# Kernel tuning notes

Hardware: AMD Instinct MI355X
Metric: run time of the kernel (lower is better)

The kernel has to match this reference:

```python
import jax, jax.numpy as jnp
import numpy as np

N, E, G = 16000, 256000, 64
H, NR, L = 128, 96, 2
CUTOFF = 6.0
EPS = 1e-10

def _ln(x, eps=1e-5):
    m = jnp.mean(x, -1, keepdims=True)
    v = jnp.mean((x - m) ** 2, -1, keepdims=True)
    return (x - m) * jax.lax.rsqrt(v + eps)

def _mlp2(x, w1, b1, w2, b2):
    return jax.nn.silu(x @ w1 + b1) @ w2 + b2

def _xav(key, shape):
    s = (2.0 / (shape[-2] + shape[-1])) ** 0.5
    return jax.random.normal(key, shape, jnp.float32) * s

def setup_inputs():
    key = jax.random.key(0)
    ks = iter(jax.random.split(key, 64))
    pos = jax.random.normal(next(ks), (N, 3), jnp.float32) * 2.0
    z = jax.random.randint(next(ks), (N,), 1, 95)
    batch = jnp.sort(jax.random.randint(next(ks), (N,), 0, G))
    src = jax.random.randint(next(ks), (E,), 0, N)
    off = jax.random.randint(next(ks), (E,), 1, N)
    dst = (src + off) % N  # no self loops -> dist > 0
    edge_index = jnp.stack([src, dst]).astype(jnp.int32)
    H3 = 3 * H
    return dict(
        pos=pos,
        z_emb_w=jax.random.normal(next(ks), (95, H), jnp.float32),
        ne_emb_w=jax.random.normal(next(ks), (95, H), jnp.float32),
        rl_w1=_xav(next(ks), (NR, H)), rl_b1=jnp.zeros((H,), jnp.float32),
        rl_w2=_xav(next(ks), (H, H)), rl_b2=jnp.zeros((H,), jnp.float32),
        sv_w=_xav(next(ks), (H, H)), sv_b=jnp.zeros((H,), jnp.float32),
        lin_w1=_xav(next(ks), (3, H // 4)), lin_b1=jnp.zeros((H // 4,), jnp.float32),
        lin_w2=_xav(next(ks), (H // 4, 1)), lin_b2=jnp.zeros((1,), jnp.float32),
        mp_ln_g=jnp.ones((L, H), jnp.float32), mp_ln_b=jnp.zeros((L, H), jnp.float32),
        mp_xw1=_xav(next(ks), (L, H, H)), mp_xb1=jnp.zeros((L, H), jnp.float32),
        mp_xw2=_xav(next(ks), (L, H, H3)), mp_xb2=jnp.zeros((L, H3), jnp.float32),
        mp_rw=_xav(next(ks), (L, NR, H3)), mp_rb=jnp.zeros((L, H3), jnp.float32),
        mp_dw1=_xav(next(ks), (L, H3 + NR, H3)), mp_db1=jnp.zeros((L, H3), jnp.float32),
        mp_dw2=_xav(next(ks), (L, H3, H3)), mp_db2=jnp.zeros((L, H3), jnp.float32),
        ft_vw=_xav(next(ks), (L, H, 2 * H)),
        ft_xw1=_xav(next(ks), (L, 2 * H, H)), ft_xb1=jnp.zeros((L, H), jnp.float32),
        ft_xw2=_xav(next(ks), (L, H, H3)), ft_xb2=jnp.zeros((L, H3), jnp.float32),
        last_w=_xav(next(ks), (H, 1)), last_b=jnp.zeros((1,), jnp.float32),
        z=z, edge_index=edge_index, batch=batch,
    )

def _forward(pos, z_emb_w, ne_emb_w, rl_w1, rl_b1, rl_w2, rl_b2, sv_w, sv_b,
             lin_w1, lin_b1, lin_w2, lin_b2, mp_ln_g, mp_ln_b, mp_xw1, mp_xb1,
             mp_xw2, mp_xb2, mp_rw, mp_rb, mp_dw1, mp_db1, mp_dw2, mp_db2,
             ft_vw, ft_xw1, ft_xb1, ft_xw2, ft_xb2, last_w, last_b,
             z, edge_index, batch):
    inv_sqrt3 = 1.0 / (3.0 ** 0.5)
    inv_sqrt_h = 1.0 / (H ** 0.5)
    inv_sqrt2 = 1.0 / (2.0 ** 0.5)
    src, dst = edge_index[0], edge_index[1]  # gather from src, scatter-add to dst
    edge_vec = pos[src] - pos[dst]                         # (E,3)
    dist = jnp.sqrt(jnp.sum(edge_vec ** 2, -1))            # (E,)
    # rbf_emb buffers
    start = jnp.exp(jnp.float32(-CUTOFF))
    means = jnp.linspace(start, 1.0, NR)
    betas = (2.0 / NR * (1.0 - start)) ** (-2.0)
    d = dist[:, None]
    rbounds = 0.5 * (jnp.cos(dist * jnp.pi / CUTOFF) + 1.0) * (dist < CUTOFF).astype(dist.dtype)
    rbf = rbounds[:, None] * jnp.exp(-betas * (jnp.exp(-d) - means) ** 2)   # (E,NR)
    rh = rbounds[:, None] * _mlp2(rbf, rl_w1, rl_b1, rl_w2, rl_b2)          # (E,H) radial_hidden
    # embeddings + NeighborEmb (gather-scale-scatter)
    s = _ln(z_emb_w[z])
    sn = _ln(ne_emb_w[z])
    s = s + jax.ops.segment_sum(rh * sn[src], dst, num_segments=N)
    vec = jnp.zeros((N, 3, H), pos.dtype)
    # edge-wise equivariant frame
    edge_diff = edge_vec / d
    edge_cross = jnp.cross(pos[src], pos[dst])
    edge_cross = edge_cross / (jnp.linalg.norm(edge_cross, axis=-1, keepdims=True) + EPS)
    edge_vertical = jnp.cross(edge_diff, edge_cross)
    edge_frame = jnp.stack([edge_diff, edge_cross, edge_vertical], -1)      # (E,3,3)
    # S_vector
    s1 = jax.nn.silu(_ln(s @ sv_w + sv_b))
    msgv = (rh[:, None, :] * edge_diff[:, :, None]) * s1[src][:, None, :]   # (E,3,H)
    S_ij = jax.ops.segment_sum(msgv, dst, num_segments=N)                   # (N,3,H)

    def _scalarize(Sg):
        sc = jnp.einsum('eck,ech->ekh', edge_frame, Sg)    # (E,3,H)
        sc = sc.at[:, 1, :].set(jnp.abs(sc[:, 1, :]))
        p = jnp.transpose(sc, (0, 2, 1))                   # (E,H,3)
        out = _mlp2(p, lin_w1, lin_b1, lin_w2, lin_b2) + p[:, :, 0:1]
        return out[..., 0]                                 # (E,H)

    scalar3 = _scalarize(S_ij[src])
    scalar4 = _scalarize(S_ij[dst])
    edge_weight = jnp.concatenate([scalar3, scalar4], -1) * rbounds[:, None]
    edge_weight = jnp.concatenate([edge_weight, rh, rbf], -1)  # (E, 3H+NR)

    for l in range(L):
        # EquiMessagePassing
        xh = _mlp2(mp_ln_g[l] * _ln(s) + mp_ln_b[l], mp_xw1[l], mp_xb1[l], mp_xw2[l], mp_xb2[l])  # (N,3H)
        rbfh = (rbf @ mp_rw[l] + mp_rb[l]) * _mlp2(edge_weight, mp_dw1[l], mp_db1[l], mp_dw2[l], mp_db2[l])
        m = xh[src] * rbfh                                  # (E,3H)
        mx, m2, m3 = jnp.split(m, 3, -1)
        m2 = m2 * inv_sqrt3
        mvec = (vec[src] * m2[:, None, :] + m3[:, None, :] * edge_diff[:, :, None]) * inv_sqrt_h
        s = (s + jax.ops.segment_sum(mx, dst, num_segments=N)) * inv_sqrt2
        vec = vec + jax.ops.segment_sum(mvec, dst, num_segments=N)
        # FTE (node_frame unused by FTE in the original code)
        vp = jnp.einsum('nch,hk->nck', vec, ft_vw[l])       # (N,3,2H)
        v1, v2 = jnp.split(vp, 2, -1)
        scalar = jnp.sqrt(jnp.sum(v1 ** 2, 1) + 1e-10)      # (N,H)
        vec_dot = jnp.sum(v1 * v2, 1) * inv_sqrt_h
        xvh = _mlp2(jnp.concatenate([s, scalar], -1), ft_xw1[l], ft_xb1[l], ft_xw2[l], ft_xb2[l])
        x1, x2, x3 = jnp.split(xvh, 3, -1)
        s = s + (x1 + x2 + vec_dot) * inv_sqrt2
        vec = vec + x3[:, None, :] * v2

    out = s @ last_w + last_b                               # (N,1)
    return jax.ops.segment_sum(out, batch, num_segments=G)  # (G,1) sum readout

def reference(pos, z_emb_w, ne_emb_w, rl_w1, rl_b1, rl_w2, rl_b2, sv_w, sv_b,
              lin_w1, lin_b1, lin_w2, lin_b2, mp_ln_g, mp_ln_b, mp_xw1, mp_xb1,
              mp_xw2, mp_xb2, mp_rw, mp_rb, mp_dw1, mp_db1, mp_dw2, mp_db2,
              ft_vw, ft_xw1, ft_xb1, ft_xw2, ft_xb2, last_w, last_b,
              z, edge_index, batch):
    return _forward(pos, z_emb_w, ne_emb_w, rl_w1, rl_b1, rl_w2, rl_b2, sv_w, sv_b,
                    lin_w1, lin_b1, lin_w2, lin_b2, mp_ln_g, mp_ln_b, mp_xw1, mp_xb1,
                    mp_xw2, mp_xb2, mp_rw, mp_rb, mp_dw1, mp_db1, mp_dw2, mp_db2,
                    ft_vw, ft_xw1, ft_xb1, ft_xw2, ft_xb2, last_w, last_b,
                    z, edge_index, batch)
```

## Files before the change

kernel.cpp:

```cpp
#include <hip/hip_runtime.h>
#include <math.h>

#define NN 16000
#define NE 256000
#define NG 64
#define HD 128
#define NRAD 96
#define H3 384
#define KD 480

typedef unsigned short u16;
typedef short short8 __attribute__((ext_vector_type(8)));
typedef float f32x4 __attribute__((ext_vector_type(4)));

__device__ __forceinline__ float siluf(float x){ return x / (1.0f + expf(-x)); }

__device__ __forceinline__ float wsum(float v){
#pragma unroll
    for (int o = 32; o > 0; o >>= 1) v += __shfl_xor(v, o, 64);
    return v;
}

__device__ __forceinline__ u16 f2bh(float f){
    unsigned int u = __float_as_uint(f);
    unsigned int r = u + 0x7FFFu + ((u >> 16) & 1u);
    return (u16)(r >> 16);
}
__device__ __forceinline__ float bh2f(u16 h){
    return __uint_as_float((unsigned int)h << 16);
}
__device__ __forceinline__ short8 ld8(const u16* p){ return *(const short8*)p; }

__global__ void k_fill(float* __restrict__ p, float v, int n){
    int i = blockIdx.x * blockDim.x + threadIdx.x;
    if (i < n) p[i] = v;
}

__global__ void k_wsplit(const float* __restrict__ src, u16* __restrict__ dh, u16* __restrict__ dl,
                         int K, int N){
    int i = blockIdx.x * 256 + threadIdx.x;
    if (i >= K * N) return;
    int n = i / K, k = i - n * K;
    float v = src[(size_t)k * N + n];
    u16 h = f2bh(v);
    dh[i] = h;
    dl[i] = f2bh(v - bh2f(h));
}

__global__ void k_node_embed(const float* __restrict__ zw, const float* __restrict__ nw,
                             const int* __restrict__ z, float* __restrict__ s, float* __restrict__ sn){
    int n = blockIdx.x, t = threadIdx.x;
    int zi = z[n];
    const float* a = zw + (size_t)zi * HD;
    const float* b = nw + (size_t)zi * HD;
    float a0 = a[t], a1 = a[t + 64];
    float m  = wsum(a0 + a1) * (1.f / HD);
    float va = wsum((a0 - m)*(a0 - m) + (a1 - m)*(a1 - m)) * (1.f / HD);
    float r  = rsqrtf(va + 1e-5f);
    s[(size_t)n*HD + t]      = (a0 - m) * r;
    s[(size_t)n*HD + 64 + t] = (a1 - m) * r;
    float b0 = b[t], b1 = b[t + 64];
    m  = wsum(b0 + b1) * (1.f / HD);
    va = wsum((b0 - m)*(b0 - m) + (b1 - m)*(b1 - m)) * (1.f / HD);
    r  = rsqrtf(va + 1e-5f);
    sn[(size_t)n*HD + t]      = (b0 - m) * r;
    sn[(size_t)n*HD + 64 + t] = (b1 - m) * r;
}

__global__ void k_ln_silu(const float* __restrict__ x, float* __restrict__ out){
    int n = blockIdx.x, t = threadIdx.x;
    float a0 = x[(size_t)n*HD + t], a1 = x[(size_t)n*HD + 64 + t];
    float m  = wsum(a0 + a1) * (1.f / HD);
    float va = wsum((a0 - m)*(a0 - m) + (a1 - m)*(a1 - m)) * (1.f / HD);
    float r  = rsqrtf(va + 1e-5f);
    out[(size_t)n*HD + t]      = siluf((a0 - m) * r);
    out[(size_t)n*HD + 64 + t] = siluf((a1 - m) * r);
}

__global__ void k_ln_aff(const float* __restrict__ x, const float* __restrict__ g,
                         const float* __restrict__ b, float* __restrict__ out){
    int n = blockIdx.x, t = threadIdx.x;
    float a0 = x[(size_t)n*HD + t], a1 = x[(size_t)n*HD + 64 + t];
    float m  = wsum(a0 + a1) * (1.f / HD);
    float va = wsum((a0 - m)*(a0 - m) + (a1 - m)*(a1 - m)) * (1.f / HD);
    float r  = rsqrtf(va + 1e-5f);
    out[(size_t)n*HD + t]      = g[t]      * ((a0 - m) * r) + b[t];
    out[(size_t)n*HD + 64 + t] = g[64 + t] * ((a1 - m) * r) + b[64 + t];
}

__global__ void k_edge_geom(const float* __restrict__ pos, const int* __restrict__ ei,
                            float* __restrict__ dist, float* __restrict__ rbnd,
                            float* __restrict__ frame){
    int e = blockIdx.x * blockDim.x + threadIdx.x;
    if (e >= NE) return;
    int si = ei[e], di = ei[NE + e];
    float sx = pos[si*3], sy = pos[si*3+1], sz = pos[si*3+2];
    float dx = pos[di*3], dy = pos[di*3+1], dz = pos[di*3+2];
    float vx = sx - dx, vy = sy - dy, vz = sz - dz;
    float dd = sqrtf(vx*vx + vy*vy + vz*vz);
    dist[e] = dd;
    float rb = (dd < 6.0f) ? 0.5f * (cosf(dd * 0.5235987755982988f) + 1.0f) : 0.0f;
    rbnd[e] = rb;
    float inv = 1.0f / dd;
    float ux = vx*inv, uy = vy*inv, uz = vz*inv;
    float cx = sy*dz - sz*dy, cy = sz*dx - sx*dz, cz = sx*dy - sy*dx;
    float cn = sqrtf(cx*cx + cy*cy + cz*cz) + 1e-10f;
    cx /= cn; cy /= cn; cz /= cn;
    float wx = uy*cz - uz*cy, wy = uz*cx - ux*cz, wz = ux*cy - uy*cx;
    frame[(0*3+0)*NE + e] = ux; frame[(1*3+0)*NE + e] = uy; frame[(2*3+0)*NE + e] = uz;
    frame[(0*3+1)*NE + e] = cx; frame[(1*3+1)*NE + e] = cy; frame[(2*3+1)*NE + e] = cz;
    frame[(0*3+2)*NE + e] = wx; frame[(1*3+2)*NE + e] = wy; frame[(2*3+2)*NE + e] = wz;
}

__global__ void k_rbf(const float* __restrict__ dist, const float* __restrict__ rbnd,
                      float* __restrict__ base, int e0, int ec){
    int idx = blockIdx.x * 256 + threadIdx.x;
    int e = idx / NRAD;
    if (e >= ec) return;
    int k = idx - e * NRAD;
    int eg = e0 + e;
    float start = expf(-6.0f);
    float mean  = start + (1.0f - start) * ((float)k / 95.0f);
    float c     = (2.0f / 96.0f) * (1.0f - start);
    float betas = 1.0f / (c * c);
    float t = expf(-dist[eg]) - mean;
    base[(size_t)e * KD + k] = rbnd[eg] * expf(-betas * t * t);
}

__global__ __launch_bounds__(256)
void mgemm(const float* __restrict__ A, int lda,
           const u16* __restrict__ Bhg, const u16* __restrict__ Blg, int K,
           const float* __restrict__ bias, int act,
           float* __restrict__ C, int ldc,
           int M, int Nn,
           const float* __restrict__ row_scale,
           const float* __restrict__ mulC, int ldm){
    __shared__ u16 Ah[128*40], Al[128*40];
    __shared__ u16 Bh[64*40],  Bl[64*40];
    int tid = threadIdx.x;
    int w = tid >> 6, l = tid & 63;
    int row0 = blockIdx.x * 128, col0 = blockIdx.y * 64;
    f32x4 acc[2][4] = {};
    const int r16 = l & 15, kb = (l >> 4) * 8;

    for (int k0 = 0; k0 < K; k0 += 32){
        if (k0) __syncthreads();
#pragma unroll
        for (int i = 0; i < 4; i++){
            int f = tid + i * 256;
            int r = f >> 3, kq = (f & 7) * 4;
            const float4 v = *(const float4*)(A + (size_t)(row0 + r) * lda + k0 + kq);
            u16 h0 = f2bh(v.x), h1 = f2bh(v.y), h2 = f2bh(v.z), h3 = f2bh(v.w);
            u16 g0 = f2bh(v.x - bh2f(h0)), g1 = f2bh(v.y - bh2f(h1));
            u16 g2 = f2bh(v.z - bh2f(h2)), g3 = f2bh(v.w - bh2f(h3));
            uint2 ph, pl;
            ph.x = (unsigned)h0 | ((unsigned)h1 << 16); ph.y = (unsigned)h2 | ((unsigned)h3 << 16);
            pl.x = (unsigned)g0 | ((unsigned)g1 << 16); pl.y = (unsigned)g2 | ((unsigned)g3 << 16);
            *(uint2*)&Ah[r*40 + kq] = ph;
            *(uint2*)&Al[r*40 + kq] = pl;
        }
        {
            int bn = tid >> 2, kq = (tid & 3) * 8;
            const size_t gb = (size_t)(col0 + bn) * K + k0 + kq;
            *(short8*)&Bh[bn*40 + kq] = ld8(Bhg + gb);
            *(short8*)&Bl[bn*40 + kq] = ld8(Blg + gb);
        }
        __syncthreads();
        short8 ah0 = *(const short8*)&Ah[(w*32      + r16)*40 + kb];
        short8 ah1 = *(const short8*)&Ah[(w*32 + 16 + r16)*40 + kb];
        short8 al0 = *(const short8*)&Al[(w*32      + r16)*40 + kb];
        short8 al1 = *(const short8*)&Al[(w*32 + 16 + r16)*40 + kb];
#pragma unroll
        for (int nf = 0; nf < 4; nf++){
            short8 bhv = *(const short8*)&Bh[(nf*16 + r16)*40 + kb];
            short8 blv = *(const short8*)&Bl[(nf*16 + r16)*40 + kb];
            acc[0][nf] = __builtin_amdgcn_mfma_f32_16x16x32_bf16(ah0, bhv, acc[0][nf], 0, 0, 0);
            acc[0][nf] = __builtin_amdgcn_mfma_f32_16x16x32_bf16(al0, bhv, acc[0][nf], 0, 0, 0);
            acc[0][nf] = __builtin_amdgcn_mfma_f32_16x16x32_bf16(ah0, blv, acc[0][nf], 0, 0, 0);
            acc[1][nf] = __builtin_amdgcn_mfma_f32_16x16x32_bf16(ah1, bhv, acc[1][nf], 0, 0, 0);
            acc[1][nf] = __builtin_amdgcn_mfma_f32_16x16x32_bf16(al1, bhv, acc[1][nf], 0, 0, 0);
            acc[1][nf] = __builtin_amdgcn_mfma_f32_16x16x32_bf16(ah1, blv, acc[1][nf], 0, 0, 0);
        }
    }
    int rq = (l >> 4) * 4;
#pragma unroll
    for (int mf = 0; mf < 2; mf++){
#pragma unroll
        for (int nf = 0; nf < 4; nf++){
            int n = col0 + nf*16 + r16;
            float bz = bias ? bias[n] : 0.0f;
#pragma unroll
            for (int reg = 0; reg < 4; reg++){
                int m = row0 + w*32 + mf*16 + rq + reg;
                float v = acc[mf][nf][reg] + bz;
                if (act) v = siluf(v);
                if (row_scale) v *= row_scale[m];
                if (mulC) v *= mulC[(size_t)m * ldm + n];
                C[(size_t)m * ldc + n] = v;
            }
        }
    }
}

struct WT { u16* h; u16* l; };

static void gemm(hipStream_t st, const float* A, int lda, WT B,
                 const float* bias, float* C, int ldc, size_t M, int K, int Nn,
                 int act, const float* rs, const float* mul, int ldm){
    dim3 g((unsigned)(M / 128), (unsigned)(Nn / 64)), b(256);
    mgemm<<<g, b, 0, st>>>(A, lda, B.h, B.l, K, bias, act, C, ldc, (int)M, Nn, rs, mul, ldm);
}

__global__ void k_scatter_s(const float* __restrict__ rh, const float* __restrict__ sn,
                            const int* __restrict__ ei, float* __restrict__ s, int e0, int ec){
    int idx = blockIdx.x * 256 + threadIdx.x;
    int e = idx >> 7, h = idx & 127;
    if (e >= ec) return;
    int eg = e0 + e;
    int si = ei[eg], di = ei[NE + eg];
    atomicAdd(&s[(size_t)di * HD + h], rh[(size_t)e * KD + h] * sn[(size_t)si * HD + h]);
}

__global__ void k_scatter_msgv(const float* __restrict__ rh, const float* __restrict__ s1,
                               const float* __restrict__ frame, const int* __restrict__ ei,
                               float* __restrict__ S_ij, int e0, int ec){
    int idx = blockIdx.x * 256 + threadIdx.x;
    int e = idx >> 7, h = idx & 127;
    if (e >= ec) return;
    int eg = e0 + e;
    int si = ei[eg], di = ei[NE + eg];
    float mv = rh[(size_t)e * KD + h] * s1[(size_t)si * HD + h];
    size_t db = (size_t)di * H3;
#pragma unroll
    for (int c = 0; c < 3; c++){
        float df = frame[(c*3 + 0) * NE + eg];
        atomicAdd(&S_ij[db + c * HD + h], mv * df);
    }
}

__global__ void k_scalarize(const float* __restrict__ S_ij, const float* __restrict__ frame,
                            const float* __restrict__ rbnd, const int* __restrict__ ei,
                            const float* __restrict__ w1, const float* __restrict__ b1,
                            const float* __restrict__ w2, const float* __restrict__ b2v,
                            float* __restrict__ base, int e0){
    int e = blockIdx.x, h = threadIdx.x;
    int eg = e0 + e;
    int si = ei[eg], di = ei[NE + eg];
    float fr[9];
#pragma unroll
    for (int i = 0; i < 9; i++) fr[i] = frame[i * NE + eg];
    float rb = rbnd[eg];
    float b2 = b2v[0];
#pragma unroll
    for (int g = 0; g < 2; g++){
        int node = g ? di : si;
        float S0 = S_ij[(size_t)node * H3 + h];
        float S1 = S_ij[(size_t)node * H3 + 128 + h];
        float S2 = S_ij[(size_t)node * H3 + 256 + h];
        float p0 = fr[0]*S0 + fr[3]*S1 + fr[6]*S2;
        float p1 = fabsf(fr[1]*S0 + fr[4]*S1 + fr[7]*S2);
        float p2 = fr[2]*S0 + fr[5]*S1 + fr[8]*S2;
        float o = b2 + p0;
#pragma unroll
        for (int j = 0; j < 32; j++){
            float hh = siluf(p0 * w1[j] + p1 * w1[32 + j] + p2 * w1[64 + j] + b1[j]);
            o += hh * w2[j];
        }
        base[(size_t)e * KD + g * 128 + h] = o * rb;
    }
}

__global__ void k_scatter_layer(const float* __restrict__ rbfh, const float* __restrict__ xh,
                                const float* __restrict__ vec, const float* __restrict__ frame,
                                const int* __restrict__ ei, float* __restrict__ s,
                                float* __restrict__ vec_acc, int e0, int ec){
    int idx = blockIdx.x * 256 + threadIdx.x;
    int e = idx >> 7, h = idx & 127;
    if (e >= ec) return;
    int eg = e0 + e;
    int si = ei[eg], di = ei[NE + eg];
    size_t eb = (size_t)e * H3, sb = (size_t)si * H3, db = (size_t)di * H3;
    float mx = xh[sb + h]       * rbfh[eb + h];
    float m2 = xh[sb + 128 + h] * rbfh[eb + 128 + h] * 0.5773502691896258f;
    float m3 = xh[sb + 256 + h] * rbfh[eb + 256 + h];
    atomicAdd(&s[(size_t)di * HD + h], mx);
#pragma unroll
    for (int c = 0; c < 3; c++){
        float df = frame[(c*3 + 0) * NE + eg];
        float mv = (vec[sb + c * HD + h] * m2 + m3 * df) * 0.08838834764831845f;
        atomicAdd(&vec_acc[db + c * HD + h], mv);
    }
}

__global__ void k_scale_s(float* __restrict__ s){
    int i = blockIdx.x * 256 + threadIdx.x;
    s[i] *= 0.7071067811865476f;
}

__global__ void k_vec_add(float* __restrict__ vec, const float* __restrict__ vec_acc){
    int i = blockIdx.x * 256 + threadIdx.x;
    vec[i] += vec_acc[i];
}

__global__ void k_vfeat(const float* __restrict__ vp, const float* __restrict__ s,
                        float* __restrict__ t256, float* __restrict__ vdot){
    int idx = blockIdx.x * 256 + threadIdx.x;
    int n = idx >> 7, h = idx & 127;
    float a = 0.f, b = 0.f;
#pragma unroll
    for (int c = 0; c < 3; c++){
        float v1 = vp[(size_t)(n*3 + c) * 256 + h];
        float v2 = vp[(size_t)(n*3 + c) * 256 + 128 + h];
        a += v1 * v1;
        b += v1 * v2;
    }
    t256[(size_t)n * 256 + 128 + h] = sqrtf(a + 1e-10f);
    vdot[idx] = b * 0.08838834764831845f;
    t256[(size_t)n * 256 + h] = s[idx];
}

__global__ void k_upd_s(float* __restrict__ s, const float* __restrict__ xvh,
                        const float* __restrict__ vdot){
    int idx = blockIdx.x * 256 + threadIdx.x;
    int n = idx >> 7, h = idx & 127;
    s[idx] += (xvh[(size_t)n * H3 + h] + xvh[(size_t)n * H3 + 128 + h] + vdot[idx]) * 0.7071067811865476f;
}

__global__ void k_upd_vec(float* __restrict__ vec, const float* __restrict__ xvh,
                          const float* __restrict__ vp){
    int idx = blockIdx.x * 256 + threadIdx.x;
    int n = idx / H3;
    int r = idx - n * H3;
    int c = r >> 7, h = r & 127;
    vec[idx] += xvh[(size_t)n * H3 + 256 + h] * vp[(size_t)(n*3 + c) * 256 + 128 + h];
}

__global__ void k_final(const float* __restrict__ s, const float* __restrict__ lw,
                        const float* __restrict__ lb, const int* __restrict__ batch,
                        float* __restrict__ out){
    int n = blockIdx.x, t = threadIdx.x;
    float v = s[(size_t)n * HD + t] * lw[t] + s[(size_t)n * HD + 64 + t] * lw[64 + t];
    v = wsum(v);
    if (t == 0) atomicAdd(&out[batch[n]], v + lb[0]);
}

extern "C" void kernel_launch(void* const* d_in, const int* in_sizes, int n_in,
                              void* d_out, int out_size, void* d_ws, size_t ws_size,
                              hipStream_t stream){
    const float* pos      = (const float*)d_in[0];
    const float* z_emb_w  = (const float*)d_in[1];
    const float* ne_emb_w = (const float*)d_in[2];
    const float* rl_w1    = (const float*)d_in[3];
    const float* rl_b1    = (const float*)d_in[4];
    const float* rl_w2    = (const float*)d_in[5];
    const float* rl_b2    = (const float*)d_in[6];
    const float* sv_w     = (const float*)d_in[7];
    const float* sv_b     = (const float*)d_in[8];
    const float* lin_w1   = (const float*)d_in[9];
    const float* lin_b1   = (const float*)d_in[10];
    const float* lin_w2   = (const float*)d_in[11];
    const float* lin_b2   = (const float*)d_in[12];
    const float* mp_ln_g  = (const float*)d_in[13];
    const float* mp_ln_b  = (const float*)d_in[14];
    const float* mp_xw1   = (const float*)d_in[15];
    const float* mp_xb1   = (const float*)d_in[16];
    const float* mp_xw2   = (const float*)d_in[17];
    const float* mp_xb2   = (const float*)d_in[18];
    const float* mp_rw    = (const float*)d_in[19];
    const float* mp_rb    = (const float*)d_in[20];
    const float* mp_dw1   = (const float*)d_in[21];
    const float* mp_db1   = (const float*)d_in[22];
    const float* mp_dw2   = (const float*)d_in[23];
    const float* mp_db2   = (const float*)d_in[24];
    const float* ft_vw    = (const float*)d_in[25];
    const float* ft_xw1   = (const float*)d_in[26];
    const float* ft_xb1   = (const float*)d_in[27];
    const float* ft_xw2   = (const float*)d_in[28];
    const float* ft_xb2   = (const float*)d_in[29];
    const float* last_w   = (const float*)d_in[30];
    const float* last_b   = (const float*)d_in[31];
    const int*   z        = (const int*)d_in[32];
    const int*   ei       = (const int*)d_in[33];
    const int*   batch    = (const int*)d_in[34];
    float* out = (float*)d_out;
    (void)in_sizes; (void)n_in; (void)out_size;

    float* ws = (float*)d_ws;
    size_t off = 0;
    auto alloc = [&](size_t nf){ float* p = ws + off; off += (nf + 63) & ~(size_t)63; return p; };

    float* s       = alloc((size_t)NN * HD);
    float* sn      = alloc((size_t)NN * HD);
    float* s1      = alloc((size_t)NN * HD);
    float* tA      = alloc((size_t)NN * HD);
    float* vdot    = alloc((size_t)NN * HD);
    float* vec     = alloc((size_t)NN * H3);
    float* vec_acc = alloc((size_t)NN * H3);
    float* S_ij    = alloc((size_t)NN * H3);
    float* xh      = alloc((size_t)NN * H3);
    float* vp      = alloc((size_t)NN * 3 * 256);
    float* dist    = alloc((size_t)NE);
    float* rbnd    = alloc((size_t)NE);
    float* frame   = alloc((size_t)NE * 9);
    float* t256    = sn;

    const size_t WELEMS = 45056 + 2 * 548864;
    u16* wcur = (u16*)alloc(WELEMS);
    auto wsplit = [&](const float* src, int K, int N)->WT{
        WT r; r.h = wcur; wcur += (size_t)K * N; r.l = wcur; wcur += (size_t)K * N;
        k_wsplit<<<(unsigned)(((size_t)K * N + 255) / 256), 256, 0, stream>>>(src, r.h, r.l, K, N);
        return r;
    };
    WT W_rl1 = wsplit(rl_w1, NRAD, HD);
    WT W_rl2 = wsplit(rl_w2, HD, HD);
    WT W_sv  = wsplit(sv_w, HD, HD);
    WT W_xw1[2], W_xw2[2], W_rw[2], W_dw1[2], W_dw2[2], W_vw[2], W_fx1[2], W_fx2[2];
    for (int l = 0; l < 2; l++){
        W_xw1[l] = wsplit(mp_xw1 + (size_t)l * HD * HD, HD, HD);
        W_xw2[l] = wsplit(mp_xw2 + (size_t)l * HD * H3, HD, H3);
        W_rw[l]  = wsplit(mp_rw  + (size_t)l * NRAD * H3, NRAD, H3);
        W_dw1[l] = wsplit(mp_dw1 + (size_t)l * KD * H3, KD, H3);
        W_dw2[l] = wsplit(mp_dw2 + (size_t)l * H3 * H3, H3, H3);
        W_vw[l]  = wsplit(ft_vw  + (size_t)l * HD * 256, HD, 256);
        W_fx1[l] = wsplit(ft_xw1 + (size_t)l * 256 * HD, 256, HD);
        W_fx2[l] = wsplit(ft_xw2 + (size_t)l * HD * H3, HD, H3);
    }

    size_t availF = ws_size / sizeof(float);
    size_t rem = (availF > off) ? (availF - off) : 0;
    const size_t EWF = (size_t)NE * KD;
    bool persist;
    size_t CE;
    float* ew  = nullptr;
    float* ewc = nullptr;
    if (rem >= EWF + 2 * (size_t)16000 * H3 + 256){
        persist = true;
        ew = alloc(EWF);
        size_t ce = (rem - EWF - 256) / (2 * (size_t)H3);
        CE = ce & ~(size_t)127;
        if (CE > NE) CE = NE;
    } else {
        persist = false;
        size_t ce = (rem > 256) ? (rem - 256) / ((size_t)KD + 2 * (size_t)H3) : 128;
        CE = ce & ~(size_t)127;
        if (CE < 128) CE = 128;
        if (CE > NE) CE = NE;
    }
    if (CE > 32768) CE = 32768;
    if (!persist) ewc = alloc(CE * KD);
    float* rbuf = alloc(CE * H3);
    float* hbuf = alloc(CE * H3);

    auto build_rh = [&](size_t e0, size_t ec, float* base){
        k_rbf<<<(unsigned)((ec * NRAD) / 256), 256, 0, stream>>>(dist, rbnd, base + 384, (int)e0, (int)ec);
        gemm(stream, base + 384, KD, W_rl1, rl_b1, hbuf, HD, ec, NRAD, HD, 1, nullptr, nullptr, 0);
        gemm(stream, hbuf, HD, W_rl2, rl_b2, base + 256, KD, ec, HD, HD, 0, rbnd + e0, nullptr, 0);
    };

    k_fill<<<1, 64, 0, stream>>>(out, 0.f, NG);
    k_node_embed<<<NN, 64, 0, stream>>>(z_emb_w, ne_emb_w, z, s, sn);
    k_edge_geom<<<NE / 256, 256, 0, stream>>>(pos, ei, dist, rbnd, frame);

    for (size_t e0 = 0; e0 < NE; e0 += CE){
        size_t ec = (NE - e0 < CE) ? (NE - e0) : CE;
        float* base = persist ? (ew + e0 * KD) : ewc;
        build_rh(e0, ec, base);
        k_scatter_s<<<(unsigned)((ec * HD) / 256), 256, 0, stream>>>(base + 256, sn, ei, s, (int)e0, (int)ec);
    }

    gemm(stream, s, HD, W_sv, sv_b, tA, HD, NN, HD, HD, 0, nullptr, nullptr, 0);
    k_ln_silu<<<NN, 64, 0, stream>>>(tA, s1);

    k_fill<<<(NN * H3) / 256, 256, 0, stream>>>(S_ij, 0.f, NN * H3);
    for (size_t e0 = 0; e0 < NE; e0 += CE){
        size_t ec = (NE - e0 < CE) ? (NE - e0) : CE;
        float* base = persist ? (ew + e0 * KD) : ewc;
        if (!persist) build_rh(e0, ec, base);
        k_scatter_msgv<<<(unsigned)((ec * HD) / 256), 256, 0, stream>>>(base + 256, s1, frame, ei, S_ij, (int)e0, (int)ec);
    }

    if (persist)
        k_scalarize<<<NE, 128, 0, stream>>>(S_ij, frame, rbnd, ei, lin_w1, lin_b1, lin_w2, lin_b2, ew, 0);

    k_fill<<<(NN * H3) / 256, 256, 0, stream>>>(vec, 0.f, NN * H3);

    for (int l = 0; l < 2; l++){
        k_ln_aff<<<NN, 64, 0, stream>>>(s, mp_ln_g + l * HD, mp_ln_b + l * HD, tA);
        gemm(stream, tA, HD, W_xw1[l], mp_xb1 + l * HD, vdot, HD, NN, HD, HD, 1, nullptr, nullptr, 0);
        gemm(stream, vdot, HD, W_xw2[l], mp_xb2 + l * H3, xh, H3, NN, HD, H3, 0, nullptr, nullptr, 0);

        k_fill<<<(NN * H3) / 256, 256, 0, stream>>>(vec_acc, 0.f, NN * H3);

        for (size_t e0 = 0; e0 < NE; e0 += CE){
            size_t ec = (NE - e0 < CE) ? (NE - e0) : CE;
            float* base = persist ? (ew + e0 * KD) : ewc;
            if (!persist){
                build_rh(e0, ec, base);
                k_scalarize<<<(unsigned)ec, 128, 0, stream>>>(S_ij, frame, rbnd, ei, lin_w1, lin_b1, lin_w2, lin_b2, base, (int)e0);
            }
            gemm(stream, base + 384, KD, W_rw[l], mp_rb + l * H3, rbuf, H3, ec, NRAD, H3, 0, nullptr, nullptr, 0);
            gemm(stream, base, KD, W_dw1[l], mp_db1 + l * H3, hbuf, H3, ec, KD, H3, 1, nullptr, nullptr, 0);
            gemm(stream, hbuf, H3, W_dw2[l], mp_db2 + l * H3, rbuf, H3, ec, H3, H3, 0, nullptr, rbuf, H3);
            k_scatter_layer<<<(unsigned)((ec * HD) / 256), 256, 0, stream>>>(rbuf, xh, vec, frame, ei, s, vec_acc, (int)e0, (int)ec);
        }
        k_scale_s<<<(NN * HD) / 256, 256, 0, stream>>>(s);
        k_vec_add<<<(NN * H3) / 256, 256, 0, stream>>>(vec, vec_acc);

        gemm(stream, vec, HD, W_vw[l], nullptr, vp, 256, (size_t)NN * 3, HD, 256, 0, nullptr, nullptr, 0);
        k_vfeat<<<(NN * HD) / 256, 256, 0, stream>>>(vp, s, t256, vdot);

        gemm(stream, t256, 256, W_fx1[l], ft_xb1 + l * HD, tA, HD, NN, 256, HD, 1, nullptr, nullptr, 0);
        gemm(stream, tA, HD, W_fx2[l], ft_xb2 + l * H3, xh, H3, NN, HD, H3, 0, nullptr, nullptr, 0);

        k_upd_s<<<(NN * HD) / 256, 256, 0, stream>>>(s, xh, vdot);
        k_upd_vec<<<(NN * H3) / 256, 256, 0, stream>>>(vec, xh, vp);
    }

    k_final<<<NN, 64, 0, stream>>>(s, last_w, last_b, batch, out);
}
```

Baseline: 12.41 ms.

## Enlarge GEMM tile to 128x128 and prefetch next K-slice into registers

The split-bf16 MFMA GEMM now uses 128x128 output tiles with a 2x2 warp layout, so each warp computes a 64x64 sub-tile of 4x4 fragments instead of 32x64. This raises MFMA work per shared-memory fragment load and halves the redundant A-tile conversion across column blocks. Global loads for the next K step are issued into registers before the current step's MFMAs, overlapping memory latency with compute. The cost is higher register pressure (64 accumulator vectors plus prefetch buffers), which may lower occupancy. Any Nn not divisible by 128 (e.g. 96) would also break.

```diff
diff --git a/kernel.cpp b/kernel.cpp
--- a/kernel.cpp
+++ b/kernel.cpp
@@ -136,62 +136,87 @@
            const float* __restrict__ row_scale,
            const float* __restrict__ mulC, int ldm){
     __shared__ u16 Ah[128*40], Al[128*40];
-    __shared__ u16 Bh[64*40],  Bl[64*40];
+    __shared__ u16 Bh[128*40], Bl[128*40];
     int tid = threadIdx.x;
     int w = tid >> 6, l = tid & 63;
-    int row0 = blockIdx.x * 128, col0 = blockIdx.y * 64;
-    f32x4 acc[2][4] = {};
-    const int r16 = l & 15, kb = (l >> 4) * 8;
-
+    int wm = w >> 1, wn = w & 1;
+    int r16 = l & 15, kb = (l >> 4) * 8, rq = (l >> 4) * 4;
+    int row0 = blockIdx.x * 128, col0 = blockIdx.y * 128;
+
+    int ar[4], akq[4];
+    const float* agp[4];
+#pragma unroll
+    for (int i = 0; i < 4; i++){
+        int f = tid + i * 256;
+        ar[i] = f >> 3; akq[i] = (f & 7) * 4;
+        agp[i] = A + (size_t)(row0 + ar[i]) * lda + akq[i];
+    }
+    int bn = tid >> 1, bkq = (tid & 1) * 16;
+    const u16* bgp_h = Bhg + (size_t)(col0 + bn) * K + bkq;
+    const u16* bgp_l = Blg + (size_t)(col0 + bn) * K + bkq;
+
+    float4 va[4];
+    short8 vbh0, vbh1, vbl0, vbl1;
+#pragma unroll
+    for (int i = 0; i < 4; i++) va[i] = *(const float4*)(agp[i]);
+    vbh0 = ld8(bgp_h); vbh1 = ld8(bgp_h + 8);
+    vbl0 = ld8(bgp_l); vbl1 = ld8(bgp_l + 8);
+
+    f32x4 acc[4][4] = {};
     for (int k0 = 0; k0 < K; k0 += 32){
         if (k0) __syncthreads();
 #pragma unroll
         for (int i = 0; i < 4; i++){
-            int f = tid + i * 256;
-            int r = f >> 3, kq = (f & 7) * 4;
-            const float4 v = *(const float4*)(A + (size_t)(row0 + r) * lda + k0 + kq);
+            float4 v = va[i];
             u16 h0 = f2bh(v.x), h1 = f2bh(v.y), h2 = f2bh(v.z), h3 = f2bh(v.w);
             u16 g0 = f2bh(v.x - bh2f(h0)), g1 = f2bh(v.y - bh2f(h1));
             u16 g2 = f2bh(v.z - bh2f(h2)), g3 = f2bh(v.w - bh2f(h3));
             uint2 ph, pl;
             ph.x = (unsigned)h0 | ((unsigned)h1 << 16); ph.y = (unsigned)h2 | ((unsigned)h3 << 16);
             pl.x = (unsigned)g0 | ((unsigned)g1 << 16); pl.y = (unsigned)g2 | ((unsigned)g3 << 16);
-            *(uint2*)&Ah[r*40 + kq] = ph;
-            *(uint2*)&Al[r*40 + kq] = pl;
-        }
-        {
-            int bn = tid >> 2, kq = (tid & 3) * 8;
-            const size_t gb = (size_t)(col0 + bn) * K + k0 + kq;
-            *(short8*)&Bh[bn*40 + kq] = ld8(Bhg + gb);
-            *(short8*)&Bl[bn*40 + kq] = ld8(Blg + gb);
-        }
+            *(uint2*)&Ah[ar[i]*40 + akq[i]] = ph;
+            *(uint2*)&Al[ar[i]*40 + akq[i]] = pl;
+        }
+        *(short8*)&Bh[bn*40 + bkq]     = vbh0;
+        *(short8*)&Bh[bn*40 + bkq + 8] = vbh1;
+        *(short8*)&Bl[bn*40 + bkq]     = vbl0;
+        *(short8*)&Bl[bn*40 + bkq + 8] = vbl1;
         __syncthreads();
-        short8 ah0 = *(const short8*)&Ah[(w*32      + r16)*40 + kb];
-        short8 ah1 = *(const short8*)&Ah[(w*32 + 16 + r16)*40 + kb];
-        short8 al0 = *(const short8*)&Al[(w*32      + r16)*40 + kb];
-        short8 al1 = *(const short8*)&Al[(w*32 + 16 + r16)*40 + kb];
+        if (k0 + 32 < K){
+#pragma unroll
+            for (int i = 0; i < 4; i++) va[i] = *(const float4*)(agp[i] + k0 + 32);
+            vbh0 = ld8(bgp_h + k0 + 32); vbh1 = ld8(bgp_h + k0 + 40);
+            vbl0 = ld8(bgp_l + k0 + 32); vbl1 = ld8(bgp_l + k0 + 40);
+        }
+        short8 fah[4], fal[4], fbh[4], fbl[4];
+#pragma unroll
+        for (int mf = 0; mf < 4; mf++){
+            fah[mf] = *(const short8*)&Ah[(wm*64 + mf*16 + r16)*40 + kb];
+            fal[mf] = *(const short8*)&Al[(wm*64 + mf*16 + r16)*40 + kb];
+        }
 #pragma unroll
         for (int nf = 0; nf < 4; nf++){
-            short8 bhv = *(const short8*)&Bh[(nf*16 + r16)*40 + kb];
-            short8 blv = *(const short8*)&Bl[(nf*16 + r16)*40 + kb];
-            acc[0][nf] = __builtin_amdgcn_mfma_f32_16x16x32_bf16(ah0, bhv, acc[0][nf], 0, 0, 0);
-            acc[0][nf] = __builtin_amdgcn_mfma_f32_16x16x32_bf16(al0, bhv, acc[0][nf], 0, 0, 0);
-            acc[0][nf] = __builtin_amdgcn_mfma_f32_16x16x32_bf16(ah0, blv, acc[0][nf], 0, 0, 0);
-            acc[1][nf] = __builtin_amdgcn_mfma_f32_16x16x32_bf16(ah1, bhv, acc[1][nf], 0, 0, 0);
-            acc[1][nf] = __builtin_amdgcn_mfma_f32_16x16x32_bf16(al1, bhv, acc[1][nf], 0, 0, 0);
-            acc[1][nf] = __builtin_amdgcn_mfma_f32_16x16x32_bf16(ah1, blv, acc[1][nf], 0, 0, 0);
-        }
-    }
-    int rq = (l >> 4) * 4;
-#pragma unroll
-    for (int mf = 0; mf < 2; mf++){
+            fbh[nf] = *(const short8*)&Bh[(wn*64 + nf*16 + r16)*40 + kb];
+            fbl[nf] = *(const short8*)&Bl[(wn*64 + nf*16 + r16)*40 + kb];
+        }
+#pragma unroll
+        for (int mf = 0; mf < 4; mf++)
+#pragma unroll
+            for (int nf = 0; nf < 4; nf++){
+                acc[mf][nf] = __builtin_amdgcn_mfma_f32_16x16x32_bf16(fah[mf], fbh[nf], acc[mf][nf], 0, 0, 0);
+                acc[mf][nf] = __builtin_amdgcn_mfma_f32_16x16x32_bf16(fal[mf], fbh[nf], acc[mf][nf], 0, 0, 0);
+                acc[mf][nf] = __builtin_amdgcn_mfma_f32_16x16x32_bf16(fah[mf], fbl[nf], acc[mf][nf], 0, 0, 0);
+            }
+    }
+#pragma unroll
+    for (int mf = 0; mf < 4; mf++){
 #pragma unroll
         for (int nf = 0; nf < 4; nf++){
-            int n = col0 + nf*16 + r16;
+            int n = col0 + wn*64 + nf*16 + r16;
             float bz = bias ? bias[n] : 0.0f;
 #pragma unroll
             for (int reg = 0; reg < 4; reg++){
-                int m = row0 + w*32 + mf*16 + rq + reg;
+                int m = row0 + wm*64 + mf*16 + rq + reg;
                 float v = acc[mf][nf][reg] + bz;
                 if (act) v = siluf(v);
                 if (row_scale) v *= row_scale[m];
@@ -207,7 +232,7 @@
 static void gemm(hipStream_t st, const float* A, int lda, WT B,
                  const float* bias, float* C, int ldc, size_t M, int K, int Nn,
                  int act, const float* rs, const float* mul, int ldm){
-    dim3 g((unsigned)(M / 128), (unsigned)(Nn / 64)), b(256);
+    dim3 g((unsigned)(M / 128), (unsigned)(Nn / 128)), b(256);
     mgemm<<<g, b, 0, st>>>(A, lda, B.h, B.l, K, bias, act, C, ldc, (int)M, Nn, rs, mul, ldm);
 }
 
```

Result: slower. 12.67 ms (+2.1%).

## Fuse radial GEMM, dw2 GEMM and edge scatter into one kernel

Applied to the files above, without the earlier changes.

Adds a kernel that computes the rbf-to-H3 GEMM and the second dense GEMM in the same tile, multiplies them with the biases, and does the atomic scatter into s and vec_acc in its epilogue. This drops the rbuf intermediate and the separate scatter kernel, removing two full edge×384 write/read round trips per chunk. Workspace sizing is reworked so chunks can grow larger without the former 32768 cap. The cost is a heavier epilogue with scattered atomics and gathers laid out per MFMA fragment, which is less coalesced than the old per-h scatter.

```diff
diff --git a/kernel.cpp b/kernel.cpp
--- a/kernel.cpp
+++ b/kernel.cpp
@@ -202,6 +202,144 @@
     }
 }
 
+__global__ __launch_bounds__(256)
+void dw2s(const float* __restrict__ hb,
+          const float* __restrict__ ewrbf,
+          const u16* __restrict__ B1h, const u16* __restrict__ B1l,
+          const u16* __restrict__ B2h, const u16* __restrict__ B2l,
+          const float* __restrict__ rb, const float* __restrict__ db2,
+          const float* __restrict__ xh, const float* __restrict__ vec,
+          const float* __restrict__ frame, const int* __restrict__ ei,
+          float* __restrict__ s, float* __restrict__ vec_acc, int e0){
+    __shared__ u16 Ah[128*40], Al[128*40];
+    __shared__ u16 Bh[64*40],  Bl[64*40];
+    int tid = threadIdx.x;
+    int w = tid >> 6, l = tid & 63;
+    int row0 = blockIdx.x * 128, col0 = blockIdx.y * 64;
+    const int r16 = l & 15, kb = (l >> 4) * 8;
+    f32x4 acc1[2][4] = {}, acc2[2][4] = {};
+
+    for (int k0 = 0; k0 < 96; k0 += 32){
+        if (k0) __syncthreads();
+#pragma unroll
+        for (int i = 0; i < 4; i++){
+            int f = tid + i * 256;
+            int r = f >> 3, kq = (f & 7) * 4;
+            const float4 v = *(const float4*)(ewrbf + (size_t)(row0 + r) * KD + k0 + kq);
+            u16 h0 = f2bh(v.x), h1 = f2bh(v.y), h2 = f2bh(v.z), h3 = f2bh(v.w);
+            u16 g0 = f2bh(v.x - bh2f(h0)), g1 = f2bh(v.y - bh2f(h1));
+            u16 g2 = f2bh(v.z - bh2f(h2)), g3 = f2bh(v.w - bh2f(h3));
+            uint2 ph, pl;
+            ph.x = (unsigned)h0 | ((unsigned)h1 << 16); ph.y = (unsigned)h2 | ((unsigned)h3 << 16);
+            pl.x = (unsigned)g0 | ((unsigned)g1 << 16); pl.y = (unsigned)g2 | ((unsigned)g3 << 16);
+            *(uint2*)&Ah[r*40 + kq] = ph;
+            *(uint2*)&Al[r*40 + kq] = pl;
+        }
+        {
+            int bn = tid >> 2, kq = (tid & 3) * 8;
+            const size_t gb = (size_t)(col0 + bn) * 96 + k0 + kq;
+            *(short8*)&Bh[bn*40 + kq] = ld8(B2h + gb);
+            *(short8*)&Bl[bn*40 + kq] = ld8(B2l + gb);
+        }
+        __syncthreads();
+        short8 ah0 = *(const short8*)&Ah[(w*32      + r16)*40 + kb];
+        short8 ah1 = *(const short8*)&Ah[(w*32 + 16 + r16)*40 + kb];
+        short8 al0 = *(const short8*)&Al[(w*32      + r16)*40 + kb];
+        short8 al1 = *(const short8*)&Al[(w*32 + 16 + r16)*40 + kb];
+#pragma unroll
+        for (int nf = 0; nf < 4; nf++){
+            short8 bhv = *(const short8*)&Bh[(nf*16 + r16)*40 + kb];
+            short8 blv = *(const short8*)&Bl[(nf*16 + r16)*40 + kb];
+            acc2[0][nf] = __builtin_amdgcn_mfma_f32_16x16x32_bf16(ah0, bhv, acc2[0][nf], 0, 0, 0);
+            acc2[0][nf] = __builtin_amdgcn_mfma_f32_16x16x32_bf16(al0, bhv, acc2[0][nf], 0, 0, 0);
+            acc2[0][nf] = __builtin_amdgcn_mfma_f32_16x16x32_bf16(ah0, blv, acc2[0][nf], 0, 0, 0);
+            acc2[1][nf] = __builtin_amdgcn_mfma_f32_16x16x32_bf16(ah1, bhv, acc2[1][nf], 0, 0, 0);
+            acc2[1][nf] = __builtin_amdgcn_mfma_f32_16x16x32_bf16(al1, bhv, acc2[1][nf], 0, 0, 0);
+            acc2[1][nf] = __builtin_amdgcn_mfma_f32_16x16x32_bf16(ah1, blv, acc2[1][nf], 0, 0, 0);
+        }
+    }
+    for (int k0 = 0; k0 < H3; k0 += 32){
+        __syncthreads();
+#pragma unroll
+        for (int i = 0; i < 4; i++){
+            int f = tid + i * 256;
+            int r = f >> 3, kq = (f & 7) * 4;
+            const float4 v = *(const float4*)(hb + (size_t)(row0 + r) * H3 + k0 + kq);
+            u16 h0 = f2bh(v.x), h1 = f2bh(v.y), h2 = f2bh(v.z), h3 = f2bh(v.w);
+            u16 g0 = f2bh(v.x - bh2f(h0)), g1 = f2bh(v.y - bh2f(h1));
+            u16 g2 = f2bh(v.z - bh2f(h2)), g3 = f2bh(v.w - bh2f(h3));
+            uint2 ph, pl;
+            ph.x = (unsigned)h0 | ((unsigned)h1 << 16); ph.y = (unsigned)h2 | ((unsigned)h3 << 16);
+            pl.x = (unsigned)g0 | ((unsigned)g1 << 16); pl.y = (unsigned)g2 | ((unsigned)g3 << 16);
+            *(uint2*)&Ah[r*40 + kq] = ph;
+            *(uint2*)&Al[r*40 + kq] = pl;
+        }
+        {
+            int bn = tid >> 2, kq = (tid & 3) * 8;
+            const size_t gb = (size_t)(col0 + bn) * H3 + k0 + kq;
+            *(short8*)&Bh[bn*40 + kq] = ld8(B1h + gb);
+            *(short8*)&Bl[bn*40 + kq] = ld8(B1l + gb);
+        }
+        __syncthreads();
+        short8 ah0 = *(const short8*)&Ah[(w*32      + r16)*40 + kb];
+        short8 ah1 = *(const short8*)&Ah[(w*32 + 16 + r16)*40 + kb];
+        short8 al0 = *(const short8*)&Al[(w*32      + r16)*40 + kb];
+        short8 al1 = *(const short8*)&Al[(w*32 + 16 + r16)*40 + kb];
+#pragma unroll
+        for (int nf = 0; nf < 4; nf++){
+            short8 bhv = *(const short8*)&Bh[(nf*16 + r16)*40 + kb];
+            short8 blv = *(const short8*)&Bl[(nf*16 + r16)*40 + kb];
+            acc1[0][nf] = __builtin_amdgcn_mfma_f32_16x16x32_bf16(ah0, bhv, acc1[0][nf], 0, 0, 0);
+            acc1[0][nf] = __builtin_amdgcn_mfma_f32_16x16x32_bf16(al0, bhv, acc1[0][nf], 0, 0, 0);
+            acc1[0][nf] = __builtin_amdgcn_mfma_f32_16x16x32_bf16(ah0, blv, acc1[0][nf], 0, 0, 0);
+            acc1[1][nf] = __builtin_amdgcn_mfma_f32_16x16x32_bf16(ah1, bhv, acc1[1][nf], 0, 0, 0);
+            acc1[1][nf] = __builtin_amdgcn_mfma_f32_16x16x32_bf16(al1, bhv, acc1[1][nf], 0, 0, 0);
+            acc1[1][nf] = __builtin_amdgcn_mfma_f32_16x16x32_bf16(ah1, blv, acc1[1][nf], 0, 0, 0);
+        }
+    }
+    int rq = (l >> 4) * 4;
+    int br = col0 >> 7;
+    int ho = col0 & 127;
+#pragma unroll
+    for (int mf = 0; mf < 2; mf++){
+#pragma unroll
+        for (int reg = 0; reg < 4; reg++){
+            int m  = row0 + w*32 + mf*16 + rq + reg;
+            int eg = e0 + m;
+            int si = ei[eg], di = ei[NE + eg];
+            float df0 = 0.f, df1 = 0.f, df2 = 0.f;
+            if (br == 2){
+                df0 = frame[0*NE + eg];
+                df1 = frame[3*NE + eg];
+                df2 = frame[6*NE + eg];
+            }
+#pragma unroll
+            for (int nf = 0; nf < 4; nf++){
+                int n = col0 + nf*16 + r16;
+                int h = ho + nf*16 + r16;
+                float v  = (acc2[mf][nf][reg] + rb[n]) * (acc1[mf][nf][reg] + db2[n]);
+                float xv = xh[(size_t)si * H3 + n];
+                if (br == 0){
+                    atomicAdd(&s[(size_t)di * HD + h], xv * v);
+                } else if (br == 1){
+                    float m2 = xv * v * 0.5773502691896258f;
+                    size_t sb = (size_t)si * H3, db = (size_t)di * H3;
+#pragma unroll
+                    for (int c = 0; c < 3; c++)
+                        atomicAdd(&vec_acc[db + c*HD + h],
+                                  vec[sb + c*HD + h] * m2 * 0.08838834764831845f);
+                } else {
+                    float m3 = xv * v * 0.08838834764831845f;
+                    size_t db = (size_t)di * H3;
+                    atomicAdd(&vec_acc[db + 0*HD + h], m3 * df0);
+                    atomicAdd(&vec_acc[db + 1*HD + h], m3 * df1);
+                    atomicAdd(&vec_acc[db + 2*HD + h], m3 * df2);
+                }
+            }
+        }
+    }
+}
+
 struct WT { u16* h; u16* l; };
 
 static void gemm(hipStream_t st, const float* A, int lda, WT B,
@@ -267,28 +405,6 @@
             o += hh * w2[j];
         }
         base[(size_t)e * KD + g * 128 + h] = o * rb;
-    }
-}
-
-__global__ void k_scatter_layer(const float* __restrict__ rbfh, const float* __restrict__ xh,
-                                const float* __restrict__ vec, const float* __restrict__ frame,
-                                const int* __restrict__ ei, float* __restrict__ s,
-                                float* __restrict__ vec_acc, int e0, int ec){
-    int idx = blockIdx.x * 256 + threadIdx.x;
-    int e = idx >> 7, h = idx & 127;
-    if (e >= ec) return;
-    int eg = e0 + e;
-    int si = ei[eg], di = ei[NE + eg];
-    size_t eb = (size_t)e * H3, sb = (size_t)si * H3, db = (size_t)di * H3;
-    float mx = xh[sb + h]       * rbfh[eb + h];
-    float m2 = xh[sb + 128 + h] * rbfh[eb + 128 + h] * 0.5773502691896258f;
-    float m3 = xh[sb + 256 + h] * rbfh[eb + 256 + h];
-    atomicAdd(&s[(size_t)di * HD + h], mx);
-#pragma unroll
-    for (int c = 0; c < 3; c++){
-        float df = frame[(c*3 + 0) * NE + eg];
-        float mv = (vec[sb + c * HD + h] * m2 + m3 * df) * 0.08838834764831845f;
-        atomicAdd(&vec_acc[db + c * HD + h], mv);
     }
 }
 
@@ -427,29 +543,29 @@
     }
 
     size_t availF = ws_size / sizeof(float);
-    size_t rem = (availF > off) ? (availF - off) : 0;
+    size_t rem = (availF > off + 1024) ? (availF - off - 1024) : 0;
     const size_t EWF = (size_t)NE * KD;
     bool persist;
     size_t CE;
     float* ew  = nullptr;
     float* ewc = nullptr;
-    if (rem >= EWF + 2 * (size_t)16000 * H3 + 256){
+    if (rem >= EWF + 128 * 384 + 256){
         persist = true;
         ew = alloc(EWF);
-        size_t ce = (rem - EWF - 256) / (2 * (size_t)H3);
+        rem = availF - off - 1024;
+        size_t ce = rem / (size_t)H3;
         CE = ce & ~(size_t)127;
+        if (CE < 128) CE = 128;
         if (CE > NE) CE = NE;
     } else {
         persist = false;
-        size_t ce = (rem > 256) ? (rem - 256) / ((size_t)KD + 2 * (size_t)H3) : 128;
+        size_t ce = rem / ((size_t)KD + (size_t)H3);
         CE = ce & ~(size_t)127;
         if (CE < 128) CE = 128;
         if (CE > NE) CE = NE;
-    }
-    if (CE > 32768) CE = 32768;
-    if (!persist) ewc = alloc(CE * KD);
-    float* rbuf = alloc(CE * H3);
-    float* hbuf = alloc(CE * H3);
+        ewc = alloc(CE * KD);
+    }
+    float* hbuf = alloc(CE * (size_t)H3);
 
     auto build_rh = [&](size_t e0, size_t ec, float* base){
         k_rbf<<<(unsigned)((ec * NRAD) / 256), 256, 0, stream>>>(dist, rbnd, base + 384, (int)e0, (int)ec);
@@ -498,10 +614,12 @@
                 build_rh(e0, ec, base);
                 k_scalarize<<<(unsigned)ec, 128, 0, stream>>>(S_ij, frame, rbnd, ei, lin_w1, lin_b1, lin_w2, lin_b2, base, (int)e0);
             }
-            gemm(stream, base + 384, KD, W_rw[l], mp_rb + l * H3, rbuf, H3, ec, NRAD, H3, 0, nullptr, nullptr, 0);
             gemm(stream, base, KD, W_dw1[l], mp_db1 + l * H3, hbuf, H3, ec, KD, H3, 1, nullptr, nullptr, 0);
-            gemm(stream, hbuf, H3, W_dw2[l], mp_db2 + l * H3, rbuf, H3, ec, H3, H3, 0, nullptr, rbuf, H3);
-            k_scatter_layer<<<(unsigned)((ec * HD) / 256), 256, 0, stream>>>(rbuf, xh, vec, frame, ei, s, vec_acc, (int)e0, (int)ec);
+            dim3 g((unsigned)(ec / 128), 6);
+            dw2s<<<g, 256, 0, stream>>>(hbuf, base + 384,
+                                        W_dw2[l].h, W_dw2[l].l, W_rw[l].h, W_rw[l].l,
+                                        mp_rb + l * H3, mp_db2 + l * H3,
+                                        xh, vec, frame, ei, s, vec_acc, (int)e0);
         }
         k_scale_s<<<(NN * HD) / 256, 256, 0, stream>>>(s);
         k_vec_add<<<(NN * H3) / 256, 256, 0, stream>>>(vec, vec_acc);
```

Result: faster. 10.70 ms (-13.8%).
